# Optimization experiments

Measured on AMD Instinct MI355X. Metric: run time of the kernel, lower is better.

The kernel has to match this reference:

```python
import jax, jax.numpy as jnp
import numpy as np

D_MODEL = 2048
NUM_HEADS = 16
D_K = D_MODEL // NUM_HEADS
THETA = 10000.0
MAX_SEQ_LEN = 2048
B, S = 2, 2048


def setup_inputs() -> dict:
    key = jax.random.key(0)
    ks = jax.random.split(key, 5)
    x = jax.random.normal(ks[0], (B, S, D_MODEL), dtype=jnp.float32)
    token_positions = jnp.tile(jnp.arange(S, dtype=jnp.int64 if jax.config.jax_enable_x64 else jnp.int32), (B, 1))
    wq = jax.random.normal(ks[1], (D_MODEL, D_MODEL), dtype=jnp.float32)
    wk = jax.random.normal(ks[2], (D_MODEL, D_MODEL), dtype=jnp.float32)
    wv = jax.random.normal(ks[3], (D_MODEL, D_MODEL), dtype=jnp.float32)
    wo = jax.random.normal(ks[4], (D_MODEL, D_MODEL), dtype=jnp.float32)
    return {"x": x, "token_positions": token_positions, "wq": wq, "wk": wk, "wv": wv, "wo": wo}


def _rope_tables():
    # inv freqs: exp(arange(0,d_k,2) * (-log(theta)/d_k))  -> [d_k/2]
    inv_freq = jnp.exp(jnp.arange(0, D_K, 2, dtype=jnp.float32) * (-np.log(THETA) / D_K))
    m = jnp.arange(MAX_SEQ_LEN, dtype=jnp.float32)[:, None]  # [L,1]
    ang = m * inv_freq[None, :]                               # [L, d_k/2]
    return jnp.cos(ang), jnp.sin(ang)


def _apply_rope(x, token_positions, cos_tab, sin_tab):
    # x: [B, H, S, d_k]; token_positions: [B, S]
    cos = cos_tab[token_positions][:, None, :, :]  # [B,1,S,d_k/2]
    sin = sin_tab[token_positions][:, None, :, :]
    xe = x[..., 0::2]
    xo = x[..., 1::2]
    re = xe * cos - xo * sin
    ro = xo * cos + xe * sin
    out = jnp.stack([re, ro], axis=-1).reshape(x.shape)
    return out


def reference(x, token_positions, wq, wk, wv, wo):
    b, s, _ = x.shape
    cos_tab, sin_tab = _rope_tables()

    def split_heads(t):  # [B,S,D] -> [B,H,S,d_k]
        return t.reshape(b, s, NUM_HEADS, D_K).transpose(0, 2, 1, 3)

    q = _apply_rope(split_heads(x @ wq), token_positions, cos_tab, sin_tab)
    k = _apply_rope(split_heads(x @ wk), token_positions, cos_tab, sin_tab)
    v = split_heads(x @ wv)

    scores = jnp.einsum("bhqd,bhkd->bhqk", q, k) / jnp.sqrt(jnp.float32(D_K))
    causal = jnp.tril(jnp.ones((s, s), dtype=bool))
    scores = jnp.where(causal[None, None], scores, jnp.float32(-1e9))
    attn = jax.nn.softmax(scores, axis=-1)
    out = jnp.einsum("bhqk,bhkd->bhqd", attn, v)
    out = out.transpose(0, 2, 1, 3).reshape(b, s, D_MODEL)
    return out @ wo
```

## Files before the change

kernel.cpp:

```cpp
#include <hip/hip_runtime.h>
#include <hip/hip_bf16.h>
#include <cstdio>

namespace {

constexpr int kSeq = 2048;
constexpr int kDModel = 2048;
constexpr int kHeads = 16;
constexpr int kDk = 128;
constexpr int kBatch = 2;
constexpr int kM = kBatch * kSeq;
constexpr float kQScale = 0.08838834764831845f;

typedef __bf16 bf16_t;
typedef __bf16 bf16x8 __attribute__((ext_vector_type(8)));
typedef __bf16 bf16x4 __attribute__((ext_vector_type(4)));
typedef float f32x4 __attribute__((ext_vector_type(4)));
typedef short s16x4 __attribute__((ext_vector_type(4)));

__device__ __forceinline__ f32x4 mfma32(bf16x8 a, bf16x8 b, f32x4 c) {
  return __builtin_amdgcn_mfma_f32_16x16x32_bf16(a, b, c, 0, 0, 0);
}

#if __has_builtin(__builtin_amdgcn_mfma_f32_16x16x16_bf16)
__device__ __forceinline__ f32x4 mfma16(bf16x4 a, bf16x4 b, f32x4 c) {
  return __builtin_amdgcn_mfma_f32_16x16x16_bf16(a, b, c, 0, 0, 0);
}
#else
__device__ __forceinline__ f32x4 mfma16(bf16x4 a, bf16x4 b, f32x4 c) {
  union U { bf16x4 b; s16x4 s; } ua, ub;
  ua.b = a; ub.b = b;
  return __builtin_amdgcn_mfma_f32_16x16x16bf16_1k(ua.s, ub.s, c, 0, 0, 0);
}
#endif

using gas_void = const __attribute__((address_space(1))) void;
using las_void = __attribute__((address_space(3))) void;

__device__ __forceinline__ void gload_lds16(const bf16_t* g, bf16_t* l) {
  __builtin_amdgcn_global_load_lds((gas_void*)g, (las_void*)l, 16, 0, 0);
}

__global__ void k_rope_table(float* __restrict__ cost, float* __restrict__ sint) {
  const int p = blockIdx.x;
  const int i = threadIdx.x;
  const double inv = exp(-(double)(2 * i) * 9.210340371976184 / 128.0);
  const double ang = (double)p * inv;
  cost[p * 64 + i] = (float)cos(ang);
  sint[p * 64 + i] = (float)sin(ang);
}

__global__ void k_split_x(const float* __restrict__ x, bf16_t* __restrict__ xh,
                          bf16_t* __restrict__ xl, int n) {
  const int idx = (blockIdx.x * blockDim.x + threadIdx.x) * 4;
  if (idx >= n) return;
  const float4 v = *(const float4*)(x + idx);
  const float vv[4] = {v.x, v.y, v.z, v.w};
  bf16x4 hv, lv;
#pragma unroll
  for (int j = 0; j < 4; ++j) {
    const bf16_t h = (bf16_t)vv[j];
    hv[j] = h;
    lv[j] = (bf16_t)(vv[j] - (float)h);
  }
  *(bf16x4*)(xh + idx) = hv;
  *(bf16x4*)(xl + idx) = lv;
}

__global__ void k_transpose_w(const float* __restrict__ w, bf16_t* __restrict__ wth,
                              bf16_t* __restrict__ wtl) {
  __shared__ float tile[32][33];
  const int bx = blockIdx.x * 32;
  const int by = blockIdx.y * 32;
  const int tx = threadIdx.x, ty = threadIdx.y;
#pragma unroll
  for (int i = 0; i < 32; i += 8)
    tile[ty + i][tx] = w[(size_t)(by + ty + i) * kDModel + bx + tx];
  __syncthreads();
#pragma unroll
  for (int i = 0; i < 32; i += 8) {
    const float v = tile[tx][ty + i];
    const size_t o = (size_t)(bx + ty + i) * kDModel + by + tx;
    const bf16_t h = (bf16_t)v;
    wth[o] = h;
    if (wtl) wtl[o] = (bf16_t)(v - (float)h);
  }
}

template <int TERMS, int EPI>
__global__ __launch_bounds__(512) void k_gemm8(
    const bf16_t* __restrict__ Ah, const bf16_t* __restrict__ Al,
    const bf16_t* __restrict__ Bh, const bf16_t* __restrict__ Bl,
    void* __restrict__ O0, void* __restrict__ O1, void* __restrict__ O2,
    void* __restrict__ O3, const int* __restrict__ tokpos,
    const float* __restrict__ cost, const float* __restrict__ sint, int NT,
    int ntk) {
  __shared__ __align__(16) bf16_t sA[3][256 * 64];
  __shared__ __align__(16) bf16_t sB[3][128 * 64];

  const int tid = threadIdx.x;
  const int wid = tid >> 6, lane = tid & 63;
  const int lo = lane & 15, hi = lane >> 4;
  const int wrr = wid >> 1, wcc = wid & 1;
  const int x7 = lo & 7;

  const int bid = blockIdx.x;
  const int wgid = (bid & 7) * (gridDim.x >> 3) + (bid >> 3);
  const int mt = wgid / NT, nt = wgid % NT;
  const int m0 = mt * 256, n0 = nt * 128;

  const int rB = tid >> 3;
  const int ch8 = ((tid & 7) ^ (rB & 7)) * 8;
  size_t offA[4], offB[2];
#pragma unroll
  for (int u = 0; u < 2; ++u)
#pragma unroll
    for (int i = 0; i < 2; ++i)
      offA[u * 2 + i] = (size_t)(m0 + u * 128 + i * 64 + rB) * 2048 + ch8;
#pragma unroll
  for (int i = 0; i < 2; ++i)
    offB[i] = (size_t)(n0 + i * 64 + rB) * 2048 + ch8;
  const int ldsOff = wid * 512;

  auto STAGE_A = [&](int slot, int t) {
    const bf16_t* base;
    if constexpr (TERMS == 3)
      base = (t < 64 ? Ah : Al) + (t & 31) * 64;
    else
      base = Ah + t * 64;
    bf16_t* d = sA[slot] + ldsOff;
#pragma unroll
    for (int ui = 0; ui < 4; ++ui) gload_lds16(base + offA[ui], d + ui * 4096);
  };
  auto STAGE_B = [&](int slot, int t) {
    const bf16_t* base;
    if constexpr (TERMS == 3)
      base = (((t >> 5) == 1) ? Bl : Bh) + (t & 31) * 64;
    else
      base = Bh + t * 64;
    bf16_t* d = sB[slot] + ldsOff;
#pragma unroll
    for (int i = 0; i < 2; ++i) gload_lds16(base + offB[i], d + i * 4096);
  };

  int aoff[4][2], boff[4][2];
#pragma unroll
  for (int mi = 0; mi < 4; ++mi)
#pragma unroll
    for (int ks = 0; ks < 2; ++ks)
      aoff[mi][ks] = (wrr * 64 + mi * 16 + lo) * 64 + (((ks * 4 + hi) ^ x7) * 8);
#pragma unroll
  for (int ni = 0; ni < 4; ++ni)
#pragma unroll
    for (int ks = 0; ks < 2; ++ks)
      boff[ni][ks] = (wcc * 64 + ni * 16 + lo) * 64 + (((ks * 4 + hi) ^ x7) * 8);

  f32x4 acc[4][4];
  const f32x4 z = {0.f, 0.f, 0.f, 0.f};
#pragma unroll
  for (int i = 0; i < 4; ++i)
#pragma unroll
    for (int j = 0; j < 4; ++j) acc[i][j] = z;

  STAGE_A(0, 0);
  STAGE_B(0, 0);
  STAGE_A(1, 1);
  STAGE_B(1, 1);
  asm volatile("s_waitcnt vmcnt(6)" ::: "memory");
  __builtin_amdgcn_s_barrier();
  asm volatile("" ::: "memory");

  int s0 = 0;
  for (int t = 0; t < ntk; ++t) {
    const bf16_t* sa = sA[s0];
    const bf16_t* sb = sB[s0];
    int s2 = s0 + 2;
    if (s2 >= 3) s2 -= 3;
    const bool pf = (t + 2 < ntk);

    bf16x8 af[2][2], bfr[4][2];
#pragma unroll
    for (int mi = 0; mi < 2; ++mi)
#pragma unroll
      for (int ks = 0; ks < 2; ++ks)
        af[mi][ks] = *(const bf16x8*)(sa + aoff[mi][ks]);
#pragma unroll
    for (int ni = 0; ni < 4; ++ni)
#pragma unroll
      for (int ks = 0; ks < 2; ++ks)
        bfr[ni][ks] = *(const bf16x8*)(sb + boff[ni][ks]);
    if (pf) STAGE_A(s2, t + 2);
    asm volatile("" ::: "memory");
    __builtin_amdgcn_s_barrier();
    asm volatile("" ::: "memory");
    __builtin_amdgcn_s_setprio(1);
#pragma unroll
    for (int ni = 0; ni < 4; ++ni)
#pragma unroll
      for (int mi = 0; mi < 2; ++mi)
#pragma unroll
        for (int ks = 0; ks < 2; ++ks)
          acc[mi][ni] = mfma32(af[mi][ks], bfr[ni][ks], acc[mi][ni]);
    __builtin_amdgcn_s_setprio(0);

    bf16x8 ag[2][2];
#pragma unroll
    for (int mi = 0; mi < 2; ++mi)
#pragma unroll
      for (int ks = 0; ks < 2; ++ks)
        ag[mi][ks] = *(const bf16x8*)(sa + aoff[2 + mi][ks]);
    if (pf) STAGE_B(s2, t + 2);
    if (pf)
      asm volatile("s_waitcnt vmcnt(6)" ::: "memory");
    else
      asm volatile("s_waitcnt vmcnt(0)" ::: "memory");
    __builtin_amdgcn_s_barrier();
    asm volatile("" ::: "memory");
    __builtin_amdgcn_s_setprio(1);
#pragma unroll
    for (int ni = 0; ni < 4; ++ni)
#pragma unroll
      for (int mi = 0; mi < 2; ++mi)
#pragma unroll
        for (int ks = 0; ks < 2; ++ks)
          acc[2 + mi][ni] = mfma32(ag[mi][ks], bfr[ni][ks], acc[2 + mi][ni]);
    __builtin_amdgcn_s_setprio(0);

    s0 += 1;
    if (s0 >= 3) s0 = 0;
  }

  if constexpr (EPI == 0) {
    float* C = (float*)O0;
#pragma unroll
    for (int mi = 0; mi < 4; ++mi)
#pragma unroll
      for (int ni = 0; ni < 4; ++ni)
#pragma unroll
        for (int r = 0; r < 4; ++r) {
          const int row = m0 + wrr * 64 + mi * 16 + hi * 4 + r;
          const int col = n0 + wcc * 64 + ni * 16 + lo;
          C[(size_t)row * 2048 + col] = acc[mi][ni][r];
        }
  } else if constexpr (EPI == 1) {
    const int qk = n0 >> 11;
    bf16_t* Xh = (bf16_t*)(qk ? O2 : O0);
    bf16_t* Xl = (bf16_t*)(qk ? O3 : O1);
    const float scale = qk ? 1.0f : kQScale;
    const int is64 = (tokpos[1] == 0) ? 1 : 0;
#pragma unroll
    for (int mi = 0; mi < 4; ++mi) {
#pragma unroll
      for (int r = 0; r < 4; ++r) {
        const int row = m0 + wrr * 64 + mi * 16 + hi * 4 + r;
        const int pos = is64 ? tokpos[2 * row] : tokpos[row];
#pragma unroll
        for (int ni = 0; ni < 4; ++ni) {
          const int col = n0 + wcc * 64 + ni * 16 + lo;
          const float v = acc[mi][ni][r] * scale;
          const float pv = __shfl_xor(v, 1);
          const int ip = (col & 127) >> 1;
          const float c = cost[pos * 64 + ip];
          const float sn = sint[pos * 64 + ip];
          const float sgn = (lo & 1) ? sn : -sn;
          const float rv = v * c + pv * sgn;
          const bf16_t hb = (bf16_t)rv;
          const size_t o = (size_t)row * 2048 + (col & 2047);
          Xh[o] = hb;
          Xl[o] = (bf16_t)(rv - (float)hb);
        }
      }
    }
  } else {
    bf16_t* VT = (bf16_t*)O0;
#pragma unroll
    for (int mi = 0; mi < 4; ++mi)
#pragma unroll
      for (int ni = 0; ni < 4; ++ni) {
        const int col = n0 + wcc * 64 + ni * 16 + lo;
        const int h = col >> 7, d = col & 127;
        const int rowb = m0 + wrr * 64 + mi * 16 + hi * 4;
        const int b = rowb >> 11, s = rowb & (kSeq - 1);
        bf16x4 ov;
#pragma unroll
        for (int r = 0; r < 4; ++r) ov[r] = (bf16_t)acc[mi][ni][r];
        *(bf16x4*)(VT + ((size_t)((b * kHeads + h) * kDk + d)) * kSeq + s) = ov;
      }
  }
}

__global__ __launch_bounds__(512, 2) void k_attn4(
    const bf16_t* __restrict__ Qh, const bf16_t* __restrict__ Ql,
    const bf16_t* __restrict__ Kh, const bf16_t* __restrict__ Kl,
    const bf16_t* __restrict__ VT, bf16_t* __restrict__ Ob) {
  __shared__ __align__(16) bf16_t sK[2][2][64 * 128];
  __shared__ __align__(16) bf16_t sV[2][128 * 64];

  const int tid = threadIdx.x;
  const int wid = tid >> 6, lane = tid & 63;
  const int lo = lane & 15, hi = lane >> 4;
  const int flat = blockIdx.x;
  const int j = flat >> 3;
  const int bh = (flat & 7) * 4 + (j & 3);
  const int p = j >> 2;
  const int b = bh >> 4, h = bh & 15;
  const int qiW = (wid < 4) ? (15 - p) : p;
  const int qw = qiW * 128 + (wid & 3) * 32;
  const int nkv = 2 * (15 - p) + 2;

  bf16x8 qhf[4][2], qlf[4][2];
  {
    const size_t qbase =
        (size_t)(b * kSeq + qw + lo) * kDModel + h * kDk + hi * 8;
#pragma unroll
    for (int qt = 0; qt < 2; ++qt)
#pragma unroll
      for (int ks = 0; ks < 4; ++ks) {
        const size_t o = qbase + (size_t)qt * 16 * kDModel + ks * 32;
        qhf[ks][qt] = *(const bf16x8*)(Qh + o);
        qlf[ks][qt] = *(const bf16x8*)(Ql + o);
      }
  }

  const int rK0 = wid * 8 + (lane >> 4);
  const int gK0 = ((lane & 15) ^ (rK0 & 15)) * 8;
  const int gK1 = ((lane & 15) ^ ((rK0 + 4) & 15)) * 8;
  const bf16_t* pKh0 = Kh + (size_t)(b * kSeq + rK0) * kDModel + h * kDk + gK0;
  const bf16_t* pKh1 = Kh + (size_t)(b * kSeq + rK0 + 4) * kDModel + h * kDk + gK1;
  const bf16_t* pKl0 = Kl + (pKh0 - Kh);
  const bf16_t* pKl1 = Kl + (pKh1 - Kh);
  const int dV0 = wid * 16 + (lane >> 3);
  const int gV0 = ((lane & 7) ^ (dV0 & 7)) * 8;
  const int gV1 = ((lane & 7) ^ ((dV0 + 8) & 7)) * 8;
  const bf16_t* pV0 = VT + (size_t)(bh * kDk + dV0) * kSeq + gV0;
  const bf16_t* pV1 = VT + (size_t)(bh * kDk + dV0 + 8) * kSeq + gV1;
  const int ldsK = (wid * 8) * 128;
  const int ldsV = (wid * 16) * 64;

  f32x4 of[8][2];
  const f32x4 z = {0.f, 0.f, 0.f, 0.f};
#pragma unroll
  for (int di = 0; di < 8; ++di) {
    of[di][0] = z;
    of[di][1] = z;
  }
  float m[2] = {-3e38f, -3e38f};
  float l[2] = {0.f, 0.f};

  auto STAGE = [&](int buf, int t) {
    const size_t ko = (size_t)t * 64 * kDModel;
    const size_t vo = (size_t)t * 64;
    bf16_t* dk = sK[buf][0] + ldsK;
    bf16_t* dl = sK[buf][1] + ldsK;
    gload_lds16(pKh0 + ko, dk);
    gload_lds16(pKh1 + ko, dk + 512);
    gload_lds16(pKl0 + ko, dl);
    gload_lds16(pKl1 + ko, dl + 512);
    bf16_t* dv = sV[buf] + ldsV;
    gload_lds16(pV0 + vo, dv);
    gload_lds16(pV1 + vo, dv + 512);
  };

  STAGE(0, 0);
  __syncthreads();

  for (int t = 0; t < nkv; ++t) {
    const int kv0 = t * 64;
    if (t + 1 < nkv) STAGE((t + 1) & 1, t + 1);

    if (kv0 <= qw + 31) {
      const bf16_t* bKh = sK[t & 1][0];
      const bf16_t* bKl = sK[t & 1][1];
      const bf16_t* bV = sV[t & 1];
      const bool maskedw = (kv0 + 63 > qw);

      f32x4 st[4][2];
#pragma unroll
      for (int kt = 0; kt < 4; ++kt) {
        st[kt][0] = z;
        st[kt][1] = z;
      }
#pragma unroll
      for (int kt = 0; kt < 4; ++kt) {
#pragma unroll
        for (int ks = 0; ks < 4; ++ks) {
          const int krow = kt * 16 + lo;
          const int ka = krow * 128 + (((ks * 4 + hi) ^ (krow & 15)) * 8);
          const bf16x8 kh8 = *(const bf16x8*)(bKh + ka);
          const bf16x8 kl8 = *(const bf16x8*)(bKl + ka);
#pragma unroll
          for (int qt = 0; qt < 2; ++qt) {
            st[kt][qt] = mfma32(kh8, qhf[ks][qt], st[kt][qt]);
            st[kt][qt] = mfma32(kh8, qlf[ks][qt], st[kt][qt]);
            st[kt][qt] = mfma32(kl8, qhf[ks][qt], st[kt][qt]);
          }
        }
      }

      bf16x4 pb[4][2];
#pragma unroll
      for (int qt = 0; qt < 2; ++qt) {
        const int q = qw + qt * 16 + lo;
        float mt = -3e38f;
#pragma unroll
        for (int kt = 0; kt < 4; ++kt)
#pragma unroll
          for (int r = 0; r < 4; ++r) {
            float s = st[kt][qt][r];
            if (maskedw && (kv0 + kt * 16 + hi * 4 + r > q)) s = -1e30f;
            st[kt][qt][r] = s;
            mt = fmaxf(mt, s);
          }
        mt = fmaxf(mt, __shfl_xor(mt, 16));
        mt = fmaxf(mt, __shfl_xor(mt, 32));
        if (!__all(mt <= m[qt] + 8.f)) {
          const float mnew = fmaxf(m[qt], mt);
          const float corr = __expf(m[qt] - mnew);
          l[qt] *= corr;
#pragma unroll
          for (int di = 0; di < 8; ++di) of[di][qt] = of[di][qt] * corr;
          m[qt] = mnew;
        }
        float rs = 0.f;
#pragma unroll
        for (int kt = 0; kt < 4; ++kt) {
          bf16x4 pv;
#pragma unroll
          for (int r = 0; r < 4; ++r) {
            const float pp = __expf(st[kt][qt][r] - m[qt]);
            rs += pp;
            pv[r] = (bf16_t)pp;
          }
          pb[kt][qt] = pv;
        }
        rs += __shfl_xor(rs, 16);
        rs += __shfl_xor(rs, 32);
        l[qt] += rs;
      }

#pragma unroll
      for (int di = 0; di < 8; ++di) {
        const int d = di * 16 + lo;
#pragma unroll
        for (int kt = 0; kt < 4; ++kt) {
          const int va =
              d * 64 + (((kt * 2 + (hi >> 1)) ^ (d & 7)) * 8) + (hi & 1) * 4;
          const bf16x4 vf = *(const bf16x4*)(bV + va);
          of[di][0] = mfma16(vf, pb[kt][0], of[di][0]);
          of[di][1] = mfma16(vf, pb[kt][1], of[di][1]);
        }
      }
    }
    __syncthreads();
  }

#pragma unroll
  for (int qt = 0; qt < 2; ++qt) {
    const float linv = 1.f / l[qt];
    const size_t ob =
        (size_t)(b * kSeq + qw + qt * 16 + lo) * kDModel + h * kDk + hi * 4;
#pragma unroll
    for (int di = 0; di < 8; ++di) {
      bf16x4 ov;
#pragma unroll
      for (int r = 0; r < 4; ++r) ov[r] = (bf16_t)(of[di][qt][r] * linv);
      *(bf16x4*)(Ob + ob + di * 16) = ov;
    }
  }
}

}

extern "C" void kernel_launch(void* const* d_in, const int* in_sizes, int n_in,
                              void* d_out, int out_size, void* d_ws, size_t ws_size,
                              hipStream_t stream) {
  (void)in_sizes; (void)n_in; (void)out_size;
  const float* x = (const float*)d_in[0];
  const int* tokpos = (const int*)d_in[1];
  const float* wq = (const float*)d_in[2];
  const float* wk = (const float*)d_in[3];
  const float* wv = (const float*)d_in[4];
  const float* wo = (const float*)d_in[5];
  float* out = (float*)d_out;

  char* p = (char*)d_ws;
  auto take = [&](size_t bytes) { char* q = p; p += bytes; return q; };
  float* cost = (float*)take((size_t)kSeq * 64 * sizeof(float));
  float* sint = (float*)take((size_t)kSeq * 64 * sizeof(float));
  const size_t mat = (size_t)kM * kDModel * sizeof(bf16_t);
  const size_t wmat = (size_t)kDModel * kDModel * sizeof(bf16_t);
  bf16_t* xh = (bf16_t*)take(mat);
  bf16_t* xl = (bf16_t*)take(mat);
  bf16_t* wqkth = (bf16_t*)take(2 * wmat);
  bf16_t* wqktl = (bf16_t*)take(2 * wmat);
  bf16_t* wvt = (bf16_t*)take(wmat);
  bf16_t* wot = (bf16_t*)take(wmat);
  bf16_t* qh = (bf16_t*)take(mat);
  bf16_t* ql = (bf16_t*)take(mat);
  bf16_t* kh = (bf16_t*)take(mat);
  bf16_t* kl = (bf16_t*)take(mat);
  bf16_t* vt = (bf16_t*)take(mat);
  bf16_t* ob = (bf16_t*)take(mat);
  if ((size_t)(p - (char*)d_ws) > ws_size) {
    fprintf(stderr, "MHA: workspace too small: need %zu have %zu\n",
            (size_t)(p - (char*)d_ws), ws_size);
    return;
  }

  k_rope_table<<<dim3(kSeq), dim3(64), 0, stream>>>(cost, sint);
  k_split_x<<<dim3((kM * kDModel) / (256 * 4)), dim3(256), 0, stream>>>(
      x, xh, xl, kM * kDModel);
  {
    dim3 tb(32, 8), tg(kDModel / 32, kDModel / 32);
    k_transpose_w<<<tg, tb, 0, stream>>>(wq, wqkth, wqktl);
    k_transpose_w<<<tg, tb, 0, stream>>>(wk, wqkth + (size_t)2048 * 2048,
                                         wqktl + (size_t)2048 * 2048);
    k_transpose_w<<<tg, tb, 0, stream>>>(wv, wvt, nullptr);
    k_transpose_w<<<tg, tb, 0, stream>>>(wo, wot, nullptr);
  }
  k_gemm8<3, 1><<<dim3(512), dim3(512), 0, stream>>>(
      xh, xl, wqkth, wqktl, qh, ql, kh, kl, tokpos, cost, sint, 32, 96);
  k_gemm8<1, 2><<<dim3(256), dim3(512), 0, stream>>>(
      xh, nullptr, wvt, nullptr, vt, nullptr, nullptr, nullptr, nullptr,
      nullptr, nullptr, 16, 32);
  k_attn4<<<dim3(256), dim3(512), 0, stream>>>(qh, ql, kh, kl, vt, ob);
  k_gemm8<1, 0><<<dim3(256), dim3(512), 0, stream>>>(
      ob, nullptr, wot, nullptr, out, nullptr, nullptr, nullptr, nullptr,
      nullptr, nullptr, 16, 32);
}
```

Baseline: 437.5 us.

## Add dedicated QK projection GEMM with 512x128 tiles and K-step 32

Replaces the templated three-term split-bf16 QK projection with a dedicated kernel that uses 512-row by 128-column tiles, a K step of 32, and 8x4 MFMA accumulators per wave. Each loaded B tile now feeds twice as many output rows, which halves the grid to 256 blocks. The staging also reorders the three precision terms (hh, hl, lh) so the full 192-step K loop runs in one pipeline. The larger register footprint (128 accumulator floats per lane) risks spills or lower occupancy, and the launch_bounds occupancy hint of 2 may not hold.

```diff
diff --git a/kernel.cpp b/kernel.cpp
--- a/kernel.cpp
+++ b/kernel.cpp
@@ -87,14 +87,145 @@
   }
 }
 
-template <int TERMS, int EPI>
-__global__ __launch_bounds__(512) void k_gemm8(
+__global__ __launch_bounds__(512, 2) void k_gemmqk(
     const bf16_t* __restrict__ Ah, const bf16_t* __restrict__ Al,
     const bf16_t* __restrict__ Bh, const bf16_t* __restrict__ Bl,
-    void* __restrict__ O0, void* __restrict__ O1, void* __restrict__ O2,
-    void* __restrict__ O3, const int* __restrict__ tokpos,
-    const float* __restrict__ cost, const float* __restrict__ sint, int NT,
-    int ntk) {
+    bf16_t* __restrict__ Qh, bf16_t* __restrict__ Ql,
+    bf16_t* __restrict__ Kh, bf16_t* __restrict__ Kl,
+    const int* __restrict__ tokpos, const float* __restrict__ cost,
+    const float* __restrict__ sint) {
+  __shared__ __align__(16) bf16_t sA[3][512 * 32];
+  __shared__ __align__(16) bf16_t sB[3][128 * 32];
+  constexpr int ntk = 192;
+
+  const int tid = threadIdx.x;
+  const int wid = tid >> 6, lane = tid & 63;
+  const int lo = lane & 15, hi = lane >> 4;
+  const int wr = wid >> 1, wc = wid & 1;
+
+  const int bid = blockIdx.x;
+  const int wgid = (bid & 7) * 32 + (bid >> 3);
+  const int mt = wgid >> 5, nt = wgid & 31;
+  const int m0 = mt * 512, n0 = nt * 128;
+
+  const int sr = tid >> 2;
+  const int sc = ((tid & 3) ^ (sr & 3)) * 8;
+  size_t offA[4];
+#pragma unroll
+  for (int ui = 0; ui < 4; ++ui)
+    offA[ui] = (size_t)(m0 + ui * 128 + sr) * 2048 + sc;
+  const size_t offB = (size_t)(n0 + sr) * 2048 + sc;
+  const int ldsT = wid * 512;
+
+  auto STAGE = [&](int slot, int tt) {
+    const bf16_t *As, *Bs;
+    int kb;
+    if (tt < 64) {
+      As = Ah; Bs = Bh; kb = tt * 32;
+    } else if (tt < 128) {
+      As = Ah; Bs = Bl; kb = (tt - 64) * 32;
+    } else {
+      As = Al; Bs = Bh; kb = (tt - 128) * 32;
+    }
+    bf16_t* dA = sA[slot] + ldsT;
+#pragma unroll
+    for (int ui = 0; ui < 4; ++ui)
+      gload_lds16(As + offA[ui] + kb, dA + ui * 4096);
+    gload_lds16(Bs + offB + kb, sB[slot] + ldsT);
+  };
+
+  int aoff[8], boff[4];
+#pragma unroll
+  for (int mi = 0; mi < 8; ++mi)
+    aoff[mi] = (wr * 128 + mi * 16 + lo) * 32 + ((hi ^ (lo & 3)) * 8);
+#pragma unroll
+  for (int ni = 0; ni < 4; ++ni)
+    boff[ni] = (wc * 64 + ni * 16 + lo) * 32 + ((hi ^ (lo & 3)) * 8);
+
+  f32x4 acc[8][4];
+  const f32x4 z = {0.f, 0.f, 0.f, 0.f};
+#pragma unroll
+  for (int i = 0; i < 8; ++i)
+#pragma unroll
+    for (int j = 0; j < 4; ++j) acc[i][j] = z;
+
+  STAGE(0, 0);
+  STAGE(1, 1);
+  asm volatile("s_waitcnt vmcnt(5)" ::: "memory");
+  __builtin_amdgcn_s_barrier();
+  __builtin_amdgcn_sched_barrier(0);
+
+  int s0 = 0;
+#pragma unroll 1
+  for (int t = 0; t < ntk; ++t) {
+    const bf16_t* sa = sA[s0];
+    const bf16_t* sb = sB[s0];
+    int s2 = s0 + 2;
+    if (s2 >= 3) s2 -= 3;
+
+    bf16x8 af[8], bfr[4];
+#pragma unroll
+    for (int mi = 0; mi < 4; ++mi) af[mi] = *(const bf16x8*)(sa + aoff[mi]);
+#pragma unroll
+    for (int ni = 0; ni < 4; ++ni) bfr[ni] = *(const bf16x8*)(sb + boff[ni]);
+    if (t + 2 < ntk) STAGE(s2, t + 2);
+#pragma unroll
+    for (int mi = 4; mi < 8; ++mi) af[mi] = *(const bf16x8*)(sa + aoff[mi]);
+
+    if (t + 3 < ntk)
+      asm volatile("s_waitcnt vmcnt(5)" ::: "memory");
+    else
+      asm volatile("s_waitcnt vmcnt(0)" ::: "memory");
+    asm volatile("s_waitcnt lgkmcnt(0)" ::: "memory");
+    __builtin_amdgcn_s_barrier();
+    __builtin_amdgcn_sched_barrier(0);
+
+    __builtin_amdgcn_s_setprio(1);
+#pragma unroll
+    for (int ni = 0; ni < 4; ++ni)
+#pragma unroll
+      for (int mi = 0; mi < 8; ++mi)
+        acc[mi][ni] = mfma32(af[mi], bfr[ni], acc[mi][ni]);
+    __builtin_amdgcn_s_setprio(0);
+
+    s0 += 1;
+    if (s0 >= 3) s0 = 0;
+  }
+
+  const int qk = n0 >> 11;
+  bf16_t* Xh = qk ? Kh : Qh;
+  bf16_t* Xl = qk ? Kl : Ql;
+  const float scale = qk ? 1.0f : kQScale;
+  const int is64 = (tokpos[1] == 0) ? 1 : 0;
+#pragma unroll
+  for (int mi = 0; mi < 8; ++mi) {
+#pragma unroll
+    for (int r = 0; r < 4; ++r) {
+      const int row = m0 + wr * 128 + mi * 16 + hi * 4 + r;
+      const int pos = is64 ? tokpos[2 * row] : tokpos[row];
+#pragma unroll
+      for (int ni = 0; ni < 4; ++ni) {
+        const int col = n0 + wc * 64 + ni * 16 + lo;
+        const float v = acc[mi][ni][r] * scale;
+        const float pv = __shfl_xor(v, 1);
+        const int ip = (col & 127) >> 1;
+        const float c = cost[pos * 64 + ip];
+        const float sn = sint[pos * 64 + ip];
+        const float sgn = (lo & 1) ? sn : -sn;
+        const float rv = v * c + pv * sgn;
+        const bf16_t hb = (bf16_t)rv;
+        const size_t o = (size_t)row * 2048 + (col & 2047);
+        Xh[o] = hb;
+        Xl[o] = (bf16_t)(rv - (float)hb);
+      }
+    }
+  }
+}
+
+template <int EPI>
+__global__ __launch_bounds__(512) void k_gemm8(
+    const bf16_t* __restrict__ Ah, const bf16_t* __restrict__ Bh,
+    void* __restrict__ O0, int NT, int ntk) {
   __shared__ __align__(16) bf16_t sA[3][256 * 64];
   __shared__ __align__(16) bf16_t sB[3][128 * 64];
 
@@ -123,21 +254,13 @@
   const int ldsOff = wid * 512;
 
   auto STAGE_A = [&](int slot, int t) {
-    const bf16_t* base;
-    if constexpr (TERMS == 3)
-      base = (t < 64 ? Ah : Al) + (t & 31) * 64;
-    else
-      base = Ah + t * 64;
+    const bf16_t* base = Ah + t * 64;
     bf16_t* d = sA[slot] + ldsOff;
 #pragma unroll
     for (int ui = 0; ui < 4; ++ui) gload_lds16(base + offA[ui], d + ui * 4096);
   };
   auto STAGE_B = [&](int slot, int t) {
-    const bf16_t* base;
-    if constexpr (TERMS == 3)
-      base = (((t >> 5) == 1) ? Bl : Bh) + (t & 31) * 64;
-    else
-      base = Bh + t * 64;
+    const bf16_t* base = Bh + t * 64;
     bf16_t* d = sB[slot] + ldsOff;
 #pragma unroll
     for (int i = 0; i < 2; ++i) gload_lds16(base + offB[i], d + i * 4096);
@@ -242,35 +365,6 @@
           const int col = n0 + wcc * 64 + ni * 16 + lo;
           C[(size_t)row * 2048 + col] = acc[mi][ni][r];
         }
-  } else if constexpr (EPI == 1) {
-    const int qk = n0 >> 11;
-    bf16_t* Xh = (bf16_t*)(qk ? O2 : O0);
-    bf16_t* Xl = (bf16_t*)(qk ? O3 : O1);
-    const float scale = qk ? 1.0f : kQScale;
-    const int is64 = (tokpos[1] == 0) ? 1 : 0;
-#pragma unroll
-    for (int mi = 0; mi < 4; ++mi) {
-#pragma unroll
-      for (int r = 0; r < 4; ++r) {
-        const int row = m0 + wrr * 64 + mi * 16 + hi * 4 + r;
-        const int pos = is64 ? tokpos[2 * row] : tokpos[row];
-#pragma unroll
-        for (int ni = 0; ni < 4; ++ni) {
-          const int col = n0 + wcc * 64 + ni * 16 + lo;
-          const float v = acc[mi][ni][r] * scale;
-          const float pv = __shfl_xor(v, 1);
-          const int ip = (col & 127) >> 1;
-          const float c = cost[pos * 64 + ip];
-          const float sn = sint[pos * 64 + ip];
-          const float sgn = (lo & 1) ? sn : -sn;
-          const float rv = v * c + pv * sgn;
-          const bf16_t hb = (bf16_t)rv;
-          const size_t o = (size_t)row * 2048 + (col & 2047);
-          Xh[o] = hb;
-          Xl[o] = (bf16_t)(rv - (float)hb);
-        }
-      }
-    }
   } else {
     bf16_t* VT = (bf16_t*)O0;
 #pragma unroll
@@ -518,13 +612,9 @@
     k_transpose_w<<<tg, tb, 0, stream>>>(wv, wvt, nullptr);
     k_transpose_w<<<tg, tb, 0, stream>>>(wo, wot, nullptr);
   }
-  k_gemm8<3, 1><<<dim3(512), dim3(512), 0, stream>>>(
-      xh, xl, wqkth, wqktl, qh, ql, kh, kl, tokpos, cost, sint, 32, 96);
-  k_gemm8<1, 2><<<dim3(256), dim3(512), 0, stream>>>(
-      xh, nullptr, wvt, nullptr, vt, nullptr, nullptr, nullptr, nullptr,
-      nullptr, nullptr, 16, 32);
+  k_gemmqk<<<dim3(256), dim3(512), 0, stream>>>(xh, xl, wqkth, wqktl, qh, ql,
+                                                kh, kl, tokpos, cost, sint);
+  k_gemm8<2><<<dim3(256), dim3(512), 0, stream>>>(xh, wvt, vt, 16, 32);
   k_attn4<<<dim3(256), dim3(512), 0, stream>>>(qh, ql, kh, kl, vt, ob);
-  k_gemm8<1, 0><<<dim3(256), dim3(512), 0, stream>>>(
-      ob, nullptr, wot, nullptr, out, nullptr, nullptr, nullptr, nullptr,
-      nullptr, nullptr, 16, 32);
-}
+  k_gemm8<0><<<dim3(256), dim3(512), 0, stream>>>(ob, wot, out, 16, 32);
+}
```

Measured after the change: 479.3 us. 9.6% more time.
